# Kernel optimization log

Measured on AMD Instinct MI355X. Metric: run time of the kernel, lower is better.

## Reference

```python
import jax, jax.numpy as jnp
import numpy as np
import jax.lax as lax

KERNEL = 7
STRIDE = 1
PAD = 3

def setup_inputs() -> dict:
    key = jax.random.key(0)
    kx, kw = jax.random.split(key)
    x = jax.random.normal(kx, (64, 512, 512), dtype=jnp.float32)
    weight = jax.random.normal(kw, (KERNEL, KERNEL), dtype=jnp.float32)
    return {"x": x, "weight": weight}

def reference(x, weight):
    # x: [B, H, W] single-channel; weight: [k, k]
    # Original computes cross-correlation (no kernel flip) with zero padding.
    lhs = x[:, None, :, :]                      # [B, 1, H, W]
    rhs = weight[None, None, :, :]              # [O=1, I=1, k, k]
    out = lax.conv_general_dilated(
        lhs, rhs,
        window_strides=(STRIDE, STRIDE),
        padding=[(PAD, PAD), (PAD, PAD)],
        dimension_numbers=("NCHW", "OIHW", "NCHW"),
    )
    return out[:, 0, :, :]                      # [B, H_out, W_out]
```

## Files before the change

### kernel.cpp

```cpp
#include <hip/hip_runtime.h>


#define IMG_W 512
#define IMG_H 512
#define NIMG  64
#define TW    256
#define TH    16
#define HALO  3
#define LDS_W 264
#define NF4   (LDS_W / 4)
#define LDS_H (TH + 2*HALO)
#define ROWP  272

__device__ __forceinline__ int swz(int c) { return c + (c >> 5); }

__global__ __launch_bounds__(256, 4) void conv7x7_kernel(
    const float* __restrict__ x,
    const float* __restrict__ wgt,
    float* __restrict__ out)
{
    __shared__ float tile[LDS_H * ROWP];

    const int tid = threadIdx.x;
    const int bx  = blockIdx.x * TW;
    const int by  = blockIdx.y * TH;
    const int n   = blockIdx.z;

    const float* img = x + (size_t)n * (IMG_W * IMG_H);

    for (int i = tid; i < LDS_H * NF4; i += 256) {
        const int r  = i / NF4;
        const int c4 = i - r * NF4;
        const int gy = by - HALO + r;
        const int gx = bx - 4 + c4 * 4;
        float4 v = make_float4(0.f, 0.f, 0.f, 0.f);
        if ((unsigned)gy < IMG_H && (unsigned)gx < IMG_W)
            v = *(const float4*)&img[gy * IMG_W + gx];
        float* rowp = &tile[r * ROWP];
        const int c = c4 * 4;
        rowp[swz(c + 0)] = v.x;
        rowp[swz(c + 1)] = v.y;
        rowp[swz(c + 2)] = v.z;
        rowp[swz(c + 3)] = v.w;
    }

    float w[49];
    #pragma unroll
    for (int i = 0; i < 49; ++i) w[i] = wgt[i];

    __syncthreads();

    const int tx = tid & 63;
    const int ty = tid >> 6;
    const int lx = tx * 4;
    const int rbase = ty * 4;

    int coff[10];
    #pragma unroll
    for (int t = 0; t < 10; ++t) coff[t] = swz(lx + 1 + t);

    float acc[4][4] = {};

    #pragma unroll
    for (int r = 0; r < 10; ++r) {
        const float* rowp = &tile[(rbase + r) * ROWP];
        float row[10];
        #pragma unroll
        for (int t = 0; t < 10; ++t) row[t] = rowp[coff[t]];
        #pragma unroll
        for (int j = 0; j < 4; ++j) {
            const int ky = r - j;
            if (ky >= 0 && ky < 7) {
                #pragma unroll
                for (int kx = 0; kx < 7; ++kx) {
                    const float wv = w[ky * 7 + kx];
                    #pragma unroll
                    for (int cc = 0; cc < 4; ++cc)
                        acc[j][cc] = fmaf(row[cc + kx], wv, acc[j][cc]);
                }
            }
        }
    }

    float* o = out + (size_t)n * (IMG_W * IMG_H);
    #pragma unroll
    for (int j = 0; j < 4; ++j) {
        float4 v = make_float4(acc[j][0], acc[j][1], acc[j][2], acc[j][3]);
        *(float4*)&o[(size_t)(by + rbase + j) * IMG_W + bx + lx] = v;
    }
}

extern "C" void kernel_launch(void* const* d_in, const int* in_sizes, int n_in,
                              void* d_out, int out_size, void* d_ws, size_t ws_size,
                              hipStream_t stream)
{
    const float* x   = (const float*)d_in[0];
    const float* wgt = (const float*)d_in[1];
    float* out       = (float*)d_out;

    dim3 grid(IMG_W / TW, IMG_H / TH, NIMG);
    conv7x7_kernel<<<grid, 256, 0, stream>>>(x, wgt, out);
}
```

Before: 125.9 us.

## Load tile interior via global_load_lds and read LDS with float4

Replaces the register-staged, swizzled tile fill with direct global-to-LDS 16-byte loads for the interior columns, using separate scalar-thread loads for the halo columns. LDS reads in the compute loop become three float4 loads per row instead of ten scalar loads, and the swizzle padding is removed. Launch bounds are raised to target 6 blocks per CU. Removing the swizzle may introduce LDS bank conflicts on the wide reads, and the direct-to-LDS path depends on the builtin's per-lane addressing semantics.

```diff
diff --git a/kernel.cpp b/kernel.cpp
--- a/kernel.cpp
+++ b/kernel.cpp
@@ -1,4 +1,5 @@
 #include <hip/hip_runtime.h>
+#include <stdint.h>
 
 
 #define IMG_W 512
@@ -8,65 +9,74 @@
 #define TH    16
 #define HALO  3
 #define LDS_W 264
-#define NF4   (LDS_W / 4)
 #define LDS_H (TH + 2*HALO)
-#define ROWP  272
 
-__device__ __forceinline__ int swz(int c) { return c + (c >> 5); }
+__device__ __forceinline__ void gload_lds16(const float* src, float* dst_lds)
+{
+    __builtin_amdgcn_global_load_lds(
+        (__attribute__((address_space(1))) void*)(uintptr_t)src,
+        (__attribute__((address_space(3))) void*)(uintptr_t)dst_lds,
+        16, 0, 0);
+}
 
-__global__ __launch_bounds__(256, 4) void conv7x7_kernel(
+__global__ __launch_bounds__(256, 6) void conv7x7_kernel(
     const float* __restrict__ x,
     const float* __restrict__ wgt,
     float* __restrict__ out)
 {
-    __shared__ float tile[LDS_H * ROWP];
+    __shared__ float tile[LDS_H * LDS_W];
 
-    const int tid = threadIdx.x;
-    const int bx  = blockIdx.x * TW;
-    const int by  = blockIdx.y * TH;
-    const int n   = blockIdx.z;
+    const int tid  = threadIdx.x;
+    const int wave = tid >> 6;
+    const int lane = tid & 63;
+    const int bx   = blockIdx.x * TW;
+    const int by   = blockIdx.y * TH;
+    const int n    = blockIdx.z;
 
     const float* img = x + (size_t)n * (IMG_W * IMG_H);
-
-    for (int i = tid; i < LDS_H * NF4; i += 256) {
-        const int r  = i / NF4;
-        const int c4 = i - r * NF4;
-        const int gy = by - HALO + r;
-        const int gx = bx - 4 + c4 * 4;
-        float4 v = make_float4(0.f, 0.f, 0.f, 0.f);
-        if ((unsigned)gy < IMG_H && (unsigned)gx < IMG_W)
-            v = *(const float4*)&img[gy * IMG_W + gx];
-        float* rowp = &tile[r * ROWP];
-        const int c = c4 * 4;
-        rowp[swz(c + 0)] = v.x;
-        rowp[swz(c + 1)] = v.y;
-        rowp[swz(c + 2)] = v.z;
-        rowp[swz(c + 3)] = v.w;
-    }
 
     float w[49];
     #pragma unroll
     for (int i = 0; i < 49; ++i) w[i] = wgt[i];
 
+    for (int r = wave; r < LDS_H; r += 4) {
+        const int gy = by - HALO + r;
+        float* dst = &tile[r * LDS_W + 4 + 4 * lane];
+        if ((unsigned)gy < IMG_H) {
+            gload_lds16(&img[(size_t)gy * IMG_W + bx + 4 * lane], dst);
+        } else {
+            *(float4*)dst = make_float4(0.f, 0.f, 0.f, 0.f);
+        }
+    }
+
+    if (tid < 2 * LDS_H) {
+        const int r    = tid >> 1;
+        const int side = tid & 1;
+        const int cb   = side ? (LDS_W - 4) : 0;
+        const int gx   = side ? (bx + 256) : (bx - 4);
+        const int gy   = by - HALO + r;
+        float4 v = make_float4(0.f, 0.f, 0.f, 0.f);
+        if (((unsigned)gy < IMG_H) && ((unsigned)gx < IMG_W))
+            v = *(const float4*)&img[(size_t)gy * IMG_W + gx];
+        *(float4*)&tile[r * LDS_W + cb] = v;
+    }
+
     __syncthreads();
 
-    const int tx = tid & 63;
-    const int ty = tid >> 6;
-    const int lx = tx * 4;
-    const int rbase = ty * 4;
-
-    int coff[10];
-    #pragma unroll
-    for (int t = 0; t < 10; ++t) coff[t] = swz(lx + 1 + t);
+    const int lx = lane * 4;
+    const int rbase = wave * 4;
 
     float acc[4][4] = {};
 
     #pragma unroll
     for (int r = 0; r < 10; ++r) {
-        const float* rowp = &tile[(rbase + r) * ROWP];
-        float row[10];
-        #pragma unroll
-        for (int t = 0; t < 10; ++t) row[t] = rowp[coff[t]];
+        const float* rowp = &tile[(rbase + r) * LDS_W + lx];
+        const float4 a = *(const float4*)(rowp + 0);
+        const float4 b = *(const float4*)(rowp + 4);
+        const float4 c = *(const float4*)(rowp + 8);
+        const float row[12] = {a.x, a.y, a.z, a.w,
+                               b.x, b.y, b.z, b.w,
+                               c.x, c.y, c.z, c.w};
         #pragma unroll
         for (int j = 0; j < 4; ++j) {
             const int ky = r - j;
@@ -76,7 +86,7 @@
                     const float wv = w[ky * 7 + kx];
                     #pragma unroll
                     for (int cc = 0; cc < 4; ++cc)
-                        acc[j][cc] = fmaf(row[cc + kx], wv, acc[j][cc]);
+                        acc[j][cc] = fmaf(row[1 + kx + cc], wv, acc[j][cc]);
                 }
             }
         }
```

New measurement: 123.9 us. About the same (-1.6%).
